# Optimization experiments

Measured on AMD Instinct MI355X. Metric: run time of the kernel, lower is better.

Reference implementation:

```python
import jax, jax.numpy as jnp
import numpy as np
import math

B, S, D_IN, D, H, L, NC = 4, 2048, 64, 512, 8, 2, 2
DK = D // H
FACTOR = 5
TOPK = min(FACTOR * int(math.log(S)), S)  # 35
EPS = 1e-5


def make_pe():
    # sinusoidal positional encoding [S, D]
    pos = jnp.arange(S, dtype=jnp.float32)[:, None]
    div = jnp.exp(jnp.arange(0, D, 2, dtype=jnp.float32) * (-math.log(10000.0) / D))
    pe = jnp.zeros((S, D), jnp.float32)
    pe = pe.at[:, 0::2].set(jnp.sin(pos * div)).at[:, 1::2].set(jnp.cos(pos * div))
    return pe


def layernorm(x, g, b):
    m = x.mean(-1, keepdims=True)
    v = x.var(-1, keepdims=True)
    return (x - m) / jnp.sqrt(v + EPS) * g + b


def setup_inputs() -> dict:
    key = jax.random.key(0)
    ks = iter(jax.random.split(key, 16))
    def p(shape, s=0.02):
        return jax.random.normal(next(ks), shape, jnp.float32) * s
    return dict(
        x=jax.random.normal(next(ks), (B, S, D_IN), jnp.float32),
        emb_w=p((D_IN, D)), emb_b=jnp.zeros((D,), jnp.float32),
        wq=p((L, D, D)), bq=jnp.zeros((L, D), jnp.float32),
        wk=p((L, D, D)), bk=jnp.zeros((L, D), jnp.float32),
        wv=p((L, D, D)), bv=jnp.zeros((L, D), jnp.float32),
        wo=p((L, D, D)), bo=jnp.zeros((L, D), jnp.float32),
        ff1_w=p((L, D, 4 * D)), ff1_b=jnp.zeros((L, 4 * D), jnp.float32),
        ff2_w=p((L, 4 * D, D)), ff2_b=jnp.zeros((L, D), jnp.float32),
        ln1_g=jnp.ones((L, D), jnp.float32), ln1_b=jnp.zeros((L, D), jnp.float32),
        ln2_g=jnp.ones((L, D), jnp.float32), ln2_b=jnp.zeros((L, D), jnp.float32),
        dec1_w=p((D, D // 2)), dec1_b=jnp.zeros((D // 2,), jnp.float32),
        dec2_w=p((D // 2, NC)), dec2_b=jnp.zeros((NC,), jnp.float32),
    )


def reference(x, emb_w, emb_b, wq, bq, wk, bk, wv, bv, wo, bo,
              ff1_w, ff1_b, ff2_w, ff2_b, ln1_g, ln1_b, ln2_g, ln2_b,
              dec1_w, dec1_b, dec2_w, dec2_b):
    h = x @ emb_w + emb_b + make_pe()[None]  # [B,S,D]
    scale = 1.0 / math.sqrt(DK)
    for i in range(L):
        q = (h @ wq[i] + bq[i]).reshape(B, S, H, DK).transpose(0, 2, 1, 3)
        k = (h @ wk[i] + bk[i]).reshape(B, S, H, DK).transpose(0, 2, 1, 3)
        v = (h @ wv[i] + bv[i]).reshape(B, S, H, DK).transpose(0, 2, 1, 3)
        scores = jnp.einsum('bhqd,bhkd->bhqk', q, k) * scale  # [B,H,S,S]
        top_scores, _ = jax.lax.top_k(scores, TOPK)            # [B,H,S,TOPK]
        attn = jax.nn.softmax(top_scores, axis=-1)
        # NOTE: faithful to source quirk — V sliced to its FIRST TOPK rows,
        # top_indices are discarded by the original module.
        ao = jnp.einsum('bhqk,bhkd->bhqd', attn, v[:, :, :TOPK, :])
        ao = ao.transpose(0, 2, 1, 3).reshape(B, S, D) @ wo[i] + bo[i]
        h = layernorm(h + ao, ln1_g[i], ln1_b[i])
        ff = jax.nn.relu(h @ ff1_w[i] + ff1_b[i]) @ ff2_w[i] + ff2_b[i]
        h = layernorm(h + ff, ln2_g[i], ln2_b[i])
    pooled = h.mean(axis=1)  # AdaptiveAvgPool1d(1) over seq
    out = jax.nn.relu(pooled @ dec1_w + dec1_b) @ dec2_w + dec2_b  # [B,NC]
    return out
```

## Files before the change

kernel.cpp:

```cpp
#include <hip/hip_runtime.h>
#include <hip/hip_bf16.h>
#include <cmath>

typedef unsigned short u16;
typedef __attribute__((ext_vector_type(8))) short short8;
typedef __attribute__((ext_vector_type(4))) float float4v;
typedef unsigned short ushort2v __attribute__((ext_vector_type(2)));

#define S_LEN 2048
#define NTOK  8192
#define TOPK  35
#define NT512 ((size_t)NTOK*512)

__device__ __forceinline__ u16 f2b(float f){
  unsigned int x = __float_as_uint(f);
  unsigned int r = (x + 0x7fffu + ((x >> 16) & 1u)) >> 16;
  return (u16)r;
}
__device__ __forceinline__ unsigned umax2(unsigned a, unsigned b){ return a > b ? a : b; }

__device__ __forceinline__ float key_to_f(unsigned key){
  unsigned m = (key & 0x8000u) ? 0x8000u : 0xFFFFu;
  return __uint_as_float(((key ^ m) & 0xFFFFu) << 16);
}
__device__ __forceinline__ unsigned pkmax(unsigned a, unsigned b){
  union { unsigned u; ushort2v v; } x, y, r;
  x.u = a; y.u = b;
  r.v = __builtin_elementwise_max(x.v, y.v);
  return r.u;
}
__device__ __forceinline__ unsigned pkmin(unsigned a, unsigned b){
  union { unsigned u; ushort2v v; } x, y, r;
  x.u = a; y.u = b;
  r.v = __builtin_elementwise_min(x.v, y.v);
  return r.u;
}

__device__ __forceinline__ void gload16(const void* g, void* l){
  __builtin_amdgcn_global_load_lds(
      (const __attribute__((address_space(1))) unsigned int*)g,
      (__attribute__((address_space(3))) unsigned int*)l, 16, 0, 0);
}

struct WtArgs {
  const float* wq; const float* wk; const float* wv; const float* wo;
  const float* ff1w; const float* ff2w;
  u16* wt_qkv; u16* wt_wo; u16* wt_ff1; u16* wt_ff2;
};
__global__ void convert_all(WtArgs a){
  __shared__ u16 t[32][33];
  int l = blockIdx.y;
  int tt = blockIdx.x;
  const float* W; u16* Wt; int K, N, tx_, ty_;
  if (tt < 1024){
    int seg = tt >> 8, r = tt & 255;
    tx_ = r & 15; ty_ = r >> 4; K = 512; N = 512;
    if (seg == 0){ W = a.wq + (size_t)l*262144; Wt = a.wt_qkv + (size_t)l*786432; }
    else if (seg == 1){ W = a.wk + (size_t)l*262144; Wt = a.wt_qkv + (size_t)l*786432 + 262144; }
    else if (seg == 2){ W = a.wv + (size_t)l*262144; Wt = a.wt_qkv + (size_t)l*786432 + 524288; }
    else { W = a.wo + (size_t)l*262144; Wt = a.wt_wo + (size_t)l*262144; }
  } else if (tt < 2048){
    int r = tt - 1024;
    tx_ = r & 63; ty_ = r >> 6; K = 512; N = 2048;
    W = a.ff1w + (size_t)l*1048576; Wt = a.wt_ff1 + (size_t)l*1048576;
  } else {
    int r = tt - 2048;
    tx_ = r & 15; ty_ = r >> 4; K = 2048; N = 512;
    W = a.ff2w + (size_t)l*1048576; Wt = a.wt_ff2 + (size_t)l*1048576;
  }
  int k0 = ty_*32, n0 = tx_*32;
  int tx = threadIdx.x, ty = threadIdx.y;
  #pragma unroll
  for (int i = ty; i < 32; i += 8)
    t[i][tx] = f2b(W[(size_t)(k0+i)*N + n0+tx]);
  __syncthreads();
  #pragma unroll
  for (int i = ty; i < 32; i += 8)
    Wt[(size_t)(n0+i)*K + k0+tx] = t[tx][i];
}

__global__ void embed_kernel(const float* __restrict__ x, const float* __restrict__ w,
                             const float* __restrict__ bias, float* __restrict__ h,
                             u16* __restrict__ h16){
  int t = blockIdx.x;
  int tid = threadIdx.x;
  __shared__ float xs[64];
  if (tid < 64) xs[tid] = x[(size_t)t*64 + tid];
  __syncthreads();
  float acc0 = bias[tid];
  float acc1 = bias[tid + 256];
  #pragma unroll 8
  for (int k = 0; k < 64; ++k){
    float xv = xs[k];
    acc0 += xv * w[k*512 + tid];
    acc1 += xv * w[k*512 + tid + 256];
  }
  int s = t & (S_LEN - 1);
  const float neg_ln1e4_over_D = -9.210340371976184f / 512.f;
  int c0 = tid, c1 = tid + 256;
  float a0 = (float)s * expf((float)(c0 & ~1) * neg_ln1e4_over_D);
  float p0 = (c0 & 1) ? cosf(a0) : sinf(a0);
  float a1 = (float)s * expf((float)(c1 & ~1) * neg_ln1e4_over_D);
  float p1 = (c1 & 1) ? cosf(a1) : sinf(a1);
  float v0 = acc0 + p0, v1 = acc1 + p1;
  h[(size_t)t*512 + c0] = v0;  h16[(size_t)t*512 + c0] = f2b(v0);
  h[(size_t)t*512 + c1] = v1;  h16[(size_t)t*512 + c1] = f2b(v1);
}

template<int EPI, int MI>
__global__ __launch_bounds__(256) void gemm_mfma(
    const u16* __restrict__ A, int lda, const u16* __restrict__ Bt, int ldb,
    const float* __restrict__ bias0, const float* __restrict__ bias1,
    const float* __restrict__ bias2,
    float* __restrict__ Cf, u16* __restrict__ C16a, u16* __restrict__ C16b,
    float* __restrict__ Cv, int M, int N, int Klen){
  __shared__ __align__(16) u16 As[MI*32*64];
  __shared__ __align__(16) u16 Bs[128*64];
  int tid = threadIdx.x;
  int w = tid >> 6, l = tid & 63, quad = l >> 4, m = l & 15;
  int m0 = blockIdx.y*(MI*32), n0 = blockIdx.x*128;
  int mh = (w >> 1)*(MI*16), nh = (w & 1)*64;
  float4v acc[MI][4];
  #pragma unroll
  for (int i = 0; i < MI; ++i)
    #pragma unroll
    for (int j = 0; j < 4; ++j) acc[i][j] = (float4v){0.f,0.f,0.f,0.f};

  for (int kt = 0; kt < Klen; kt += 64){
    #pragma unroll
    for (int c = 0; c < MI; ++c){
      int g = c*256 + tid;
      int row = g >> 3, sc = g & 7, dc = sc ^ (row & 7);
      gload16(A + (size_t)(m0+row)*lda + kt + dc*8, As + (size_t)g*8);
    }
    #pragma unroll
    for (int c = 0; c < 4; ++c){
      int g = c*256 + tid;
      int row = g >> 3, sc = g & 7, dc = sc ^ (row & 7);
      gload16(Bt + (size_t)(n0+row)*ldb + kt + dc*8, Bs + (size_t)g*8);
    }
    __syncthreads();
    #pragma unroll
    for (int kk = 0; kk < 2; ++kk){
      short8 af[MI], bf[4];
      #pragma unroll
      for (int i = 0; i < MI; ++i){
        int dcx = kk*4 + quad;
        int ra = mh + i*16 + m;
        af[i] = *(const short8*)(As + (size_t)(ra*8 + (dcx ^ (ra & 7)))*8);
      }
      #pragma unroll
      for (int j = 0; j < 4; ++j){
        int dcx = kk*4 + quad;
        int rb = nh + j*16 + m;
        bf[j] = *(const short8*)(Bs + (size_t)(rb*8 + (dcx ^ (rb & 7)))*8);
      }
      #pragma unroll
      for (int i = 0; i < MI; ++i)
        #pragma unroll
        for (int j = 0; j < 4; ++j)
          acc[i][j] = __builtin_amdgcn_mfma_f32_16x16x32_bf16(af[i], bf[j], acc[i][j], 0, 0, 0);
    }
    __syncthreads();
  }

  #pragma unroll
  for (int i = 0; i < MI; ++i){
    #pragma unroll
    for (int j = 0; j < 4; ++j){
      int col = n0 + nh + j*16 + m;
      #pragma unroll
      for (int r = 0; r < 4; ++r){
        int row = m0 + mh + i*16 + quad*4 + r;
        float v = acc[i][j][r];
        if (EPI == 0){
          Cf[(size_t)row*N + col] = v + bias0[col];
        } else if (EPI == 1){
          C16a[(size_t)row*N + col] = f2b(fmaxf(v + bias0[col], 0.f));
        } else {
          int sel = col >> 9, n5 = col & 511;
          const float* bp = (sel == 0) ? bias0 : (sel == 1) ? bias1 : bias2;
          float vv = v + bp[n5];
          int d = n5 & 63, hh = n5 >> 6;
          int b = row >> 11, s = row & 2047;
          size_t idx = (((size_t)(b*8 + hh))*2048 + s)*64 + d;
          if (sel == 0)      C16a[idx] = f2b(vv);
          else if (sel == 1) C16b[idx] = f2b(vv);
          else               Cv[idx]  = vv;
        }
      }
    }
  }
}

__global__ __launch_bounds__(512) void attn_mfma_topk(
    const u16* __restrict__ qb16, const u16* __restrict__ kb16,
    const float* __restrict__ vb, u16* __restrict__ aob16){
  __shared__ unsigned pr[8*2048];
  int tid  = threadIdx.x;
  int w    = tid >> 6, l = tid & 63;
  int quad = l >> 4,  m = l & 15;
  int bh = blockIdx.y;
  int q0 = blockIdx.x * 16;

  const u16* Qp = qb16 + ((size_t)bh*2048 + q0 + m)*64 + quad*8;
  short8 a0 = *(const short8*)Qp;
  short8 a1 = *(const short8*)(Qp + 32);

  const u16* Kbase = kb16 + (size_t)bh*2048*64;
  for (int kt = 0; kt < 16; ++kt){
    int k0 = w*256 + kt*16;
    const u16* Kp = Kbase + (size_t)(k0 + m)*64 + quad*8;
    short8 b0 = *(const short8*)Kp;
    short8 b1 = *(const short8*)(Kp + 32);
    float4v acc = {0.f, 0.f, 0.f, 0.f};
    acc = __builtin_amdgcn_mfma_f32_16x16x32_bf16(a0, b0, acc, 0, 0, 0);
    acc = __builtin_amdgcn_mfma_f32_16x16x32_bf16(a1, b1, acc, 0, 0, 0);
    #pragma unroll
    for (int c = 0; c < 2; ++c){
      union { __hip_bfloat162 b; unsigned u; } cv;
      cv.b = __float22bfloat162_rn(float2{acc[2*c], acc[2*c+1]});
      unsigned neg = (cv.u >> 15) & 0x00010001u;
      pr[(quad*2 + c)*2048 + k0 + m] = cv.u ^ (0x80008000u | (neg * 0x7FFFu));
    }
  }
  __syncthreads();

  unsigned* row = &pr[w*2048];

  unsigned sc[32];
  const uint4* p4 = (const uint4*)row;
  #pragma unroll
  for (int j = 0; j < 8; ++j){
    uint4 v4 = p4[j*64 + l];
    sc[j*4+0] = v4.x; sc[j*4+1] = v4.y; sc[j*4+2] = v4.z; sc[j*4+3] = v4.w;
  }

  #pragma unroll
  for (int k = 2; k <= 32; k <<= 1){
    #pragma unroll
    for (int j = k >> 1; j > 0; j >>= 1){
      #pragma unroll
      for (int i = 0; i < 32; ++i){
        int ixj = i ^ j;
        if (ixj > i){
          unsigned a = sc[i], b = sc[ixj];
          unsigned hi = pkmax(a, b), lo = pkmin(a, b);
          if ((i & k) == 0){ sc[i] = hi; sc[ixj] = lo; }
          else             { sc[i] = lo; sc[ixj] = hi; }
        }
      }
    }
  }

  #pragma unroll
  for (int i = 0; i < 32; ++i) row[i*64 + l] = sc[i];

  unsigned headA = sc[0] & 0xFFFFu, headB = sc[0] >> 16;
  unsigned nxtA  = sc[1] & 0xFFFFu, nxtB  = sc[1] >> 16;
  int pA = 0, pB = 0;
  unsigned tvP[TOPK];
  #pragma unroll
  for (int r = 0; r < TOPK; r += 2){
    unsigned m1 = headA | (headB << 16);
    unsigned m2 = 0;
    #pragma unroll
    for (int off = 32; off > 0; off >>= 1){
      unsigned o1 = __shfl_xor(m1, off, 64);
      unsigned o2 = __shfl_xor(m2, off, 64);
      unsigned lo = pkmin(m1, o1);
      m1 = pkmax(m1, o1);
      m2 = pkmax(pkmax(m2, o2), lo);
    }
    tvP[r] = m1;
    unsigned mA = m1 & 0xFFFFu, mB = m1 >> 16;
    int ownA = __ffsll(__ballot(headA == mA)) - 1;
    if (l == ownA){ headA = nxtA; ++pA; }
    int ownB = __ffsll(__ballot(headB == mB)) - 1;
    if (l == ownB){ headB = nxtB; ++pB; }
    nxtA = (pA + 1 < 32) ? (row[(pA + 1)*64 + l] & 0xFFFFu) : 0u;
    nxtB = (pB + 1 < 32) ? (row[(pB + 1)*64 + l] >> 16)     : 0u;
    if (r + 1 < TOPK){
      unsigned nA = (unsigned)__shfl((int)headA, ownA, 64);
      unsigned nB = (unsigned)__shfl((int)headB, ownB, 64);
      unsigned cA = umax2(m2 & 0xFFFFu, nA);
      unsigned cB = umax2(m2 >> 16, nB);
      tvP[r + 1] = cA | (cB << 16);
      int o2A = __ffsll(__ballot(headA == cA)) - 1;
      if (l == o2A){ headA = nxtA; ++pA; }
      int o2B = __ffsll(__ballot(headB == cB)) - 1;
      if (l == o2B){ headB = nxtB; ++pB; }
      nxtA = (pA + 1 < 32) ? (row[(pA + 1)*64 + l] & 0xFFFFu) : 0u;
      nxtB = (pB + 1 < 32) ? (row[(pB + 1)*64 + l] >> 16)     : 0u;
    }
  }

  const float* Vb = vb + (size_t)bh*2048*64 + l;
  float vreg[TOPK];
  #pragma unroll
  for (int r = 0; r < TOPK; ++r) vreg[r] = Vb[(size_t)r*64];
  int b = bh >> 3, hh = bh & 7;
  #pragma unroll
  for (int which = 0; which < 2; ++which){
    float tv[TOPK];
    #pragma unroll
    for (int r = 0; r < TOPK; ++r){
      unsigned key = which ? (tvP[r] >> 16) : (tvP[r] & 0xFFFFu);
      tv[r] = key_to_f(key) * 0.125f;
    }
    float mx = tv[0], denom = 0.f, acc = 0.f;
    #pragma unroll
    for (int r = 0; r < TOPK; ++r){
      float e = __expf(tv[r] - mx);
      denom += e;
      acc += e * vreg[r];
    }
    acc /= denom;
    int s = q0 + w*2 + which;
    aob16[(((size_t)(b*2048 + s))*8 + hh)*64 + l] = f2b(acc);
  }
}

__global__ void resid_ln_kernel(float* __restrict__ h, const float* __restrict__ t,
                                const float* __restrict__ g, const float* __restrict__ b,
                                u16* __restrict__ h16){
  int tok = blockIdx.x;
  int tid = threadIdx.x;
  size_t base = (size_t)tok * 512;
  float x0 = h[base + tid]       + t[base + tid];
  float x1 = h[base + tid + 256] + t[base + tid + 256];
  __shared__ float red[8];
  int wid = tid >> 6, lane = tid & 63;

  float s = x0 + x1;
  #pragma unroll
  for (int off = 32; off > 0; off >>= 1) s += __shfl_xor(s, off, 64);
  if (lane == 0) red[wid] = s;
  __syncthreads();
  float mean = (red[0] + red[1] + red[2] + red[3]) * (1.f/512.f);

  float d0 = x0 - mean, d1 = x1 - mean;
  float sq = d0*d0 + d1*d1;
  #pragma unroll
  for (int off = 32; off > 0; off >>= 1) sq += __shfl_xor(sq, off, 64);
  if (lane == 0) red[4 + wid] = sq;
  __syncthreads();
  float var = (red[4] + red[5] + red[6] + red[7]) * (1.f/512.f);
  float inv = rsqrtf(var + 1e-5f);
  float o0 = d0 * inv * g[tid]       + b[tid];
  float o1 = d1 * inv * g[tid + 256] + b[tid + 256];
  h[base + tid]         = o0;  h16[base + tid]       = f2b(o0);
  h[base + tid + 256]   = o1;  h16[base + tid + 256] = f2b(o1);
}

__global__ void pool_zero(float* __restrict__ pooled){
  pooled[blockIdx.x*512 + threadIdx.x] = 0.f;
}
__global__ void pool_kernel(const float* __restrict__ h, float* __restrict__ pooled){
  int c = blockIdx.x * 256 + threadIdx.x;
  int b = blockIdx.y;
  int s0 = blockIdx.z * 64;
  const float* p = h + ((size_t)b * 2048 + s0) * 512 + c;
  float acc = 0.f;
  #pragma unroll 8
  for (int s = 0; s < 64; ++s) acc += p[(size_t)s * 512];
  atomicAdd(&pooled[b*512 + c], acc * (1.f/2048.f));
}

__global__ void decoder_kernel(const float* __restrict__ pooled,
                               const float* __restrict__ w1, const float* __restrict__ b1,
                               const float* __restrict__ w2, const float* __restrict__ b2,
                               float* __restrict__ out){
  __shared__ float ps[4][512];
  __shared__ float hid[4][256];
  int tid = threadIdx.x;
  for (int i = tid; i < 2048; i += 256) ps[i >> 9][i & 511] = pooled[i];
  __syncthreads();
  float bb = b1[tid];
  for (int b = 0; b < 4; ++b){
    float acc = bb;
    for (int k = 0; k < 512; ++k) acc += ps[b][k] * w1[k*256 + tid];
    hid[b][tid] = fmaxf(acc, 0.f);
  }
  __syncthreads();
  if (tid < 8){
    int b = tid >> 1, c = tid & 1;
    float acc = b2[c];
    for (int j = 0; j < 256; ++j) acc += hid[b][j] * w2[j*2 + c];
    out[b*2 + c] = acc;
  }
}

extern "C" void kernel_launch(void* const* d_in, const int* in_sizes, int n_in,
                              void* d_out, int out_size, void* d_ws, size_t ws_size,
                              hipStream_t stream){
  const float* x     = (const float*)d_in[0];
  const float* emb_w = (const float*)d_in[1];
  const float* emb_b = (const float*)d_in[2];
  const float* wq    = (const float*)d_in[3];
  const float* bq    = (const float*)d_in[4];
  const float* wk    = (const float*)d_in[5];
  const float* bk    = (const float*)d_in[6];
  const float* wv    = (const float*)d_in[7];
  const float* bv    = (const float*)d_in[8];
  const float* wo    = (const float*)d_in[9];
  const float* bo    = (const float*)d_in[10];
  const float* ff1w  = (const float*)d_in[11];
  const float* ff1b  = (const float*)d_in[12];
  const float* ff2w  = (const float*)d_in[13];
  const float* ff2b  = (const float*)d_in[14];
  const float* ln1g  = (const float*)d_in[15];
  const float* ln1b  = (const float*)d_in[16];
  const float* ln2g  = (const float*)d_in[17];
  const float* ln2b  = (const float*)d_in[18];
  const float* d1w   = (const float*)d_in[19];
  const float* d1b   = (const float*)d_in[20];
  const float* d2w   = (const float*)d_in[21];
  const float* d2b   = (const float*)d_in[22];

  float* h      = (float*)d_ws;
  float* tmp    = h + NT512;
  u16*   u      = (u16*)(tmp + NT512);
  u16*   h16    = u;
  u16*   q16    = u + NT512;
  u16*   k16    = u + 2*NT512;
  float* vb     = (float*)(u + 3*NT512);
  u16*   ff16   = q16;
  u16*   aob16  = (u16*)(vb + NT512);
  u16*   wt     = aob16 + NT512;
  u16*   wt_qkv = wt;
  u16*   wt_wo  = wt_qkv + (size_t)2*1536*512;
  u16*   wt_ff1 = wt_wo  + (size_t)2*512*512;
  u16*   wt_ff2 = wt_ff1 + (size_t)2*2048*512;
  float* pooled = (float*)(wt_ff2 + (size_t)2*512*2048);

  WtArgs wa{wq, wk, wv, wo, ff1w, ff2w, wt_qkv, wt_wo, wt_ff1, wt_ff2};
  convert_all<<<dim3(3072, 2), dim3(32, 8), 0, stream>>>(wa);

  embed_kernel<<<NTOK, 256, 0, stream>>>(x, emb_w, emb_b, h, h16);

  for (int l = 0; l < 2; ++l){
    gemm_mfma<2,4><<<dim3(12, 64), 256, 0, stream>>>(
        h16, 512, wt_qkv + (size_t)l*1536*512, 512,
        bq + l*512, bk + l*512, bv + l*512,
        nullptr, q16, k16, vb, NTOK, 1536, 512);

    attn_mfma_topk<<<dim3(128, 32), 512, 0, stream>>>(q16, k16, vb, aob16);

    gemm_mfma<0,2><<<dim3(4, 128), 256, 0, stream>>>(
        aob16, 512, wt_wo + (size_t)l*512*512, 512,
        bo + l*512, nullptr, nullptr,
        tmp, nullptr, nullptr, nullptr, NTOK, 512, 512);
    resid_ln_kernel<<<NTOK, 256, 0, stream>>>(h, tmp, ln1g + l*512, ln1b + l*512, h16);

    gemm_mfma<1,4><<<dim3(16, 64), 256, 0, stream>>>(
        h16, 512, wt_ff1 + (size_t)l*2048*512, 512,
        ff1b + l*2048, nullptr, nullptr,
        nullptr, ff16, nullptr, nullptr, NTOK, 2048, 512);

    gemm_mfma<0,2><<<dim3(4, 128), 256, 0, stream>>>(
        ff16, 2048, wt_ff2 + (size_t)l*512*2048, 2048,
        ff2b + l*512, nullptr, nullptr,
        tmp, nullptr, nullptr, nullptr, NTOK, 512, 2048);
    resid_ln_kernel<<<NTOK, 256, 0, stream>>>(h, tmp, ln2g + l*512, ln2b + l*512, h16);
  }

  pool_zero<<<4, 512, 0, stream>>>(pooled);
  pool_kernel<<<dim3(2, 4, 32), 256, 0, stream>>>(h, pooled);
  decoder_kernel<<<1, 256, 0, stream>>>(pooled, d1w, d1b, d2w, d2b, (float*)d_out);
}
```

Measured before the change: 842.7 us.

## Compute only the needed V rows, skew attention LDS, enlarge output GEMM tiles

The QKV projection now skips V for all but the first 128 rows of each batch, since attention only reads the first TOPK rows of V. Blocks covering the rest of the V columns return early. The attention score scratch writes are rotated per row to cut LDS bank conflicts; this is safe because top-k selection does not depend on element order within a row. The Wo and FF2 GEMMs use larger M tiles (MI=4), and pooled zeroing is folded into the weight-conversion kernel to drop one launch. Risks: larger tiles give fewer blocks and less occupancy, and V beyond row 128 is left unwritten.

Measured after the change: 918.4 us. 1.09x slower.

```diff
diff --git a/kernel.cpp b/kernel.cpp
--- a/kernel.cpp
+++ b/kernel.cpp
@@ -46,11 +46,17 @@
   const float* wq; const float* wk; const float* wv; const float* wo;
   const float* ff1w; const float* ff2w;
   u16* wt_qkv; u16* wt_wo; u16* wt_ff1; u16* wt_ff2;
+  float* pooled;
 };
 __global__ void convert_all(WtArgs a){
   __shared__ u16 t[32][33];
   int l = blockIdx.y;
   int tt = blockIdx.x;
+  if (tt == 0 && l == 0){
+    int th = threadIdx.y*32 + threadIdx.x;
+    #pragma unroll
+    for (int i = 0; i < 8; ++i) a.pooled[i*256 + th] = 0.f;
+  }
   const float* W; u16* Wt; int K, N, tx_, ty_;
   if (tt < 1024){
     int seg = tt >> 8, r = tt & 255;
@@ -114,11 +120,17 @@
     const float* __restrict__ bias2,
     float* __restrict__ Cf, u16* __restrict__ C16a, u16* __restrict__ C16b,
     float* __restrict__ Cv, int M, int N, int Klen){
+  bool vpath = false;
+  if (EPI == 2 && blockIdx.x >= 8){
+    if (blockIdx.y >= 4) return;
+    vpath = true;
+  }
   __shared__ __align__(16) u16 As[MI*32*64];
   __shared__ __align__(16) u16 Bs[128*64];
   int tid = threadIdx.x;
   int w = tid >> 6, l = tid & 63, quad = l >> 4, m = l & 15;
-  int m0 = blockIdx.y*(MI*32), n0 = blockIdx.x*128;
+  int m0 = vpath ? blockIdx.y*2048 : blockIdx.y*(MI*32);
+  int n0 = blockIdx.x*128;
   int mh = (w >> 1)*(MI*16), nh = (w & 1)*64;
   float4v acc[MI][4];
   #pragma unroll
@@ -171,22 +183,29 @@
       int col = n0 + nh + j*16 + m;
       #pragma unroll
       for (int r = 0; r < 4; ++r){
-        int row = m0 + mh + i*16 + quad*4 + r;
+        int rl  = mh + i*16 + quad*4 + r;
+        int row = m0 + rl;
         float v = acc[i][j][r];
         if (EPI == 0){
           Cf[(size_t)row*N + col] = v + bias0[col];
         } else if (EPI == 1){
           C16a[(size_t)row*N + col] = f2b(fmaxf(v + bias0[col], 0.f));
         } else {
-          int sel = col >> 9, n5 = col & 511;
-          const float* bp = (sel == 0) ? bias0 : (sel == 1) ? bias1 : bias2;
-          float vv = v + bp[n5];
-          int d = n5 & 63, hh = n5 >> 6;
-          int b = row >> 11, s = row & 2047;
-          size_t idx = (((size_t)(b*8 + hh))*2048 + s)*64 + d;
-          if (sel == 0)      C16a[idx] = f2b(vv);
-          else if (sel == 1) C16b[idx] = f2b(vv);
-          else               Cv[idx]  = vv;
+          if (!vpath){
+            int sel = col >> 9, n5 = col & 511;
+            float vv = v + (sel ? bias1[n5] : bias0[n5]);
+            int d = n5 & 63, hh = n5 >> 6;
+            int b = row >> 11, s = row & 2047;
+            size_t idx = (((size_t)(b*8 + hh))*2048 + s)*64 + d;
+            if (sel == 0) C16a[idx] = f2b(vv);
+            else          C16b[idx] = f2b(vv);
+          } else {
+            int colv = col - 1024;
+            float vv = v + bias2[colv];
+            int d = colv & 63, hh = colv >> 6;
+            size_t idx = (((size_t)(blockIdx.y*8 + hh))*2048 + rl)*64 + d;
+            Cv[idx] = vv;
+          }
         }
       }
     }
@@ -221,7 +240,8 @@
       union { __hip_bfloat162 b; unsigned u; } cv;
       cv.b = __float22bfloat162_rn(float2{acc[2*c], acc[2*c+1]});
       unsigned neg = (cv.u >> 15) & 0x00010001u;
-      pr[(quad*2 + c)*2048 + k0 + m] = cv.u ^ (0x80008000u | (neg * 0x7FFFu));
+      int prow = quad*2 + c;
+      pr[prow*2048 + ((k0 + m + prow*4) & 2047)] = cv.u ^ (0x80008000u | (neg * 0x7FFFu));
     }
   }
   __syncthreads();
@@ -353,9 +373,6 @@
   h[base + tid + 256]   = o1;  h16[base + tid + 256] = f2b(o1);
 }
 
-__global__ void pool_zero(float* __restrict__ pooled){
-  pooled[blockIdx.x*512 + threadIdx.x] = 0.f;
-}
 __global__ void pool_kernel(const float* __restrict__ h, float* __restrict__ pooled){
   int c = blockIdx.x * 256 + threadIdx.x;
   int b = blockIdx.y;
@@ -434,7 +451,7 @@
   u16*   wt_ff2 = wt_ff1 + (size_t)2*2048*512;
   float* pooled = (float*)(wt_ff2 + (size_t)2*512*2048);
 
-  WtArgs wa{wq, wk, wv, wo, ff1w, ff2w, wt_qkv, wt_wo, wt_ff1, wt_ff2};
+  WtArgs wa{wq, wk, wv, wo, ff1w, ff2w, wt_qkv, wt_wo, wt_ff1, wt_ff2, pooled};
   convert_all<<<dim3(3072, 2), dim3(32, 8), 0, stream>>>(wa);
 
   embed_kernel<<<NTOK, 256, 0, stream>>>(x, emb_w, emb_b, h, h16);
@@ -443,11 +460,11 @@
     gemm_mfma<2,4><<<dim3(12, 64), 256, 0, stream>>>(
         h16, 512, wt_qkv + (size_t)l*1536*512, 512,
         bq + l*512, bk + l*512, bv + l*512,
-        nullptr, q16, k16, vb, NTOK, 1536, 512);
+        nullptr, q16, k16, vb, NTOK, 1024, 512);
 
     attn_mfma_topk<<<dim3(128, 32), 512, 0, stream>>>(q16, k16, vb, aob16);
 
-    gemm_mfma<0,2><<<dim3(4, 128), 256, 0, stream>>>(
+    gemm_mfma<0,4><<<dim3(4, 64), 256, 0, stream>>>(
         aob16, 512, wt_wo + (size_t)l*512*512, 512,
         bo + l*512, nullptr, nullptr,
         tmp, nullptr, nullptr, nullptr, NTOK, 512, 512);
@@ -458,14 +475,13 @@
         ff1b + l*2048, nullptr, nullptr,
         nullptr, ff16, nullptr, nullptr, NTOK, 2048, 512);
 
-    gemm_mfma<0,2><<<dim3(4, 128), 256, 0, stream>>>(
+    gemm_mfma<0,4><<<dim3(4, 64), 256, 0, stream>>>(
         ff16, 2048, wt_ff2 + (size_t)l*512*2048, 2048,
         ff2b + l*512, nullptr, nullptr,
         tmp, nullptr, nullptr, nullptr, NTOK, 512, 2048);
     resid_ln_kernel<<<NTOK, 256, 0, stream>>>(h, tmp, ln2g + l*512, ln2b + l*512, h16);
   }
 
-  pool_zero<<<4, 512, 0, stream>>>(pooled);
   pool_kernel<<<dim3(2, 4, 32), 256, 0, stream>>>(h, pooled);
   decoder_kernel<<<1, 256, 0, stream>>>(pooled, d1w, d1b, d2w, d2b, (float*)d_out);
 }
```
